# Optimization experiments

Measured on AMD Instinct MI355X. Metric: run time of the kernel, lower is better.

The kernel has to match this reference:

```python
import jax, jax.numpy as jnp
import numpy as np

KSIZE = 31
PAD = KSIZE // 2  # 15
SIGMA = 6.0
GAMMA_0 = 1.0
GAMMA_DELTA = 0.6
THRESH = 55.0


def _gabor_kernels(theta, freq):
    """Per-pixel spatially-varying Gabor kernels.
    theta, freq: [N] -> kernels [N, KSIZE, KSIZE].
    Frequency is chirped along the wave axis by freq_delta = freq/3 and the
    Gaussian aspect ratio varies from gamma_0 at the center by gamma_delta
    toward the kernel edge (matches generate_custom_gabor_torch semantics).
    """
    half = KSIZE // 2
    r = jnp.arange(-half, half + 1, dtype=jnp.float32)
    yy, xx = jnp.meshgrid(r, r, indexing='ij')  # [K,K]
    ct = jnp.cos(theta)[:, None, None]
    st = jnp.sin(theta)[:, None, None]
    x_t = xx * ct + yy * st       # along-wave coordinate
    y_t = -xx * st + yy * ct      # across-wave coordinate
    f0 = freq[:, None, None]
    f_local = f0 + (f0 / 3.0) * (y_t / half)          # freq_delta = freq/3
    gamma = GAMMA_0 + GAMMA_DELTA * jnp.abs(y_t) / half
    env = jnp.exp(-(x_t ** 2 + (gamma * y_t) ** 2) / (2.0 * SIGMA ** 2))
    return env * jnp.cos(2.0 * jnp.pi * f_local * x_t)


def _gabor_forward(fprint, freq_map, theta_map):
    H, W = fprint.shape
    i0, i1 = PAD, H - 16          # loop bounds: range(15, H-16)
    j0, j1 = PAD, W - 16
    Hout, Wout = i1 - i0, j1 - j0  # H-31, W-31 (patches always fully in-bounds)

    # [K*K, H-30, W-30] im2col patches; valid-output index 0 is center PAD.
    patches = jax.lax.conv_general_dilated_patches(
        fprint[None, None], (KSIZE, KSIZE), (1, 1), 'VALID')[0]
    patches = patches[:, :Hout, :Wout]  # centers i0..i1-1, j0..j1-1

    theta = theta_map[i0:i1, j0:j1].astype(jnp.float32) / 180.0 * jnp.pi
    freq = 0.025 + 0.0015 * freq_map[i0:i1, j0:j1].astype(jnp.float32)
    kernels = _gabor_kernels(theta.reshape(-1), freq.reshape(-1))
    kernels = kernels.reshape(Hout, Wout, KSIZE * KSIZE)

    vals = jnp.einsum('khw,hwk->hw', patches, kernels)
    out = fprint.at[i0:i1, j0:j1].set(vals)

    # normalize2Df_print_torch: shift min to 0, scale max to 100
    out = out - jnp.min(out)
    mx = jnp.max(out)
    out = jnp.where(mx != 0, out / mx * 100.0, out)
    # binarize2Df_print_torch
    return jnp.where(out > THRESH, 100.0, 0.0)


def setup_inputs() -> dict:
    key = jax.random.key(0)
    k1, k2, k3 = jax.random.split(key, 3)
    H = W = 320
    fprint = jax.random.uniform(k1, (H, W), dtype=jnp.float32) * 100.0
    freq_map = jax.random.randint(k2, (H, W), 0, 20, dtype=jnp.int32)
    theta_map = jax.random.randint(k3, (H, W), 0, 180, dtype=jnp.int32)
    return {"fprint": fprint, "freq_map": freq_map, "theta_map": theta_map}


def reference(fprint, freq_map, theta_map):
    return _gabor_forward(fprint, freq_map, theta_map)
```

## Files before the change

### kernel.cpp

```cpp
#include <hip/hip_runtime.h>
#include <math.h>

#define KS    31
#define KSP   32
#define PADV  15
#define IMG   320
#define NOUT  289
#define NTH   180
#define TABQ  (KSP * KSP)

#define PBX   4
#define PBY   2
#define TROWS (PBY + KSP - 1)
#define TSTR  37
#define NSTG  (TROWS * TSTR)
#define GX    73
#define GY    145
#define NPART (GX * GY)
#define NBORD 18879

typedef float f32x4 __attribute__((ext_vector_type(4)));

__global__ __launch_bounds__(256) void build_eftab(float2* __restrict__ tab) {
    const int t = blockIdx.x >> 2;
    const int e = (blockIdx.x & 3) * 256 + threadIdx.x;
    const float th = ((float)t / 180.0f) * 3.14159265358979323846f;
    float st, ct;
    sincosf(th, &st, &ct);
    int dy = e >> 5, dx = e & 31;
    float2 v = make_float2(0.0f, 0.0f);
    if (dy < KS && dx < KS) {
        float y = (float)(dy - PADV);
        float x = (float)(dx - PADV);
        float x_t = fmaf(x,  ct, y * st);
        float y_t = fmaf(-x, st, y * ct);
        float gamma = fmaf(0.04f, fabsf(y_t), 1.0f);
        float gyt = gamma * y_t;
        float env = expf(-fmaf(x_t, x_t, gyt * gyt) * (1.0f / 72.0f));
        float phi = fmaf(x_t * y_t, (1.0f / 45.0f), x_t);
        v = make_float2(env, phi);
    }
    tab[(size_t)t * TABQ + e] = v;
}

__global__ __launch_bounds__(256, 4) void gabor_conv(
    const float* __restrict__ fp, const int* __restrict__ fmap,
    const int* __restrict__ tmap, const float2* __restrict__ tab,
    float* __restrict__ out, float2* __restrict__ part)
{
    __shared__ float tile[NSTG];
    __shared__ float smin[8], smax[8];
    const int bh = blockIdx.y * PBY;
    const int bw = blockIdx.x * PBX;
    const int tid = threadIdx.x;

    const int wave = tid >> 6, lane = tid & 63;
    const int half = lane >> 5, l = lane & 31;
    const int lr = l & 15, lh = l >> 4;
    const int pb  = wave * 2 + half;
    const int pxl = pb & 3, pyl = pb >> 2;
    const int oy = bh + pyl, ox = bw + pxl;
    const bool valid = (oy < NOUT) && (ox < NOUT);

    f32x4 g0a, g0b, g0c, g0d, g1a, g1b, g1c, g1d;
    f32x4 g2a, g2b, g2c, g2d, g3a, g3b, g3c, g3d;
    float f0 = 0.0f;
    unsigned long long a = 0;

#define ISSUE(R0,R1,R2,R3,A,O0,O1,O2,O3) asm volatile(                        \
        "global_load_dwordx4 %0, %4, off offset:" #O0 "\n\t"                  \
        "global_load_dwordx4 %1, %4, off offset:" #O1 "\n\t"                  \
        "global_load_dwordx4 %2, %4, off offset:" #O2 "\n\t"                  \
        "global_load_dwordx4 %3, %4, off offset:" #O3                         \
        : "=&v"(R0), "=&v"(R1), "=&v"(R2), "=&v"(R3) : "v"(A) : "memory")
#define WAITTIE(N,R0,R1,R2,R3)                                                \
        asm volatile("s_waitcnt vmcnt(" #N ")"                                \
            : "+v"(R0), "+v"(R1), "+v"(R2), "+v"(R3) :: "memory");            \
        __builtin_amdgcn_sched_barrier(0)
#define WAITTIE8(R0,R1,R2,R3,R4,R5,R6,R7)                                     \
        asm volatile("s_waitcnt vmcnt(8)"                                     \
            : "+v"(R0), "+v"(R1), "+v"(R2), "+v"(R3),                         \
              "+v"(R4), "+v"(R5), "+v"(R6), "+v"(R7) :: "memory");            \
        __builtin_amdgcn_sched_barrier(0)
#define COMP(W, i) { const float* tr_ = tbase + 2 * (i) * TSTR;               \
        float w0_ = W.x * __builtin_amdgcn_cosf(f0 * W.y);                    \
        float w1_ = W.z * __builtin_amdgcn_cosf(f0 * W.w);                    \
        acc0 = fmaf(tr_[0], w0_, acc0); acc1 = fmaf(tr_[1], w1_, acc1); }

    if (valid) {
        const int iy = oy + PADV, ix = ox + PADV;
        const int theta = tmap[iy * IMG + ix];
        f0 = 0.025f + 0.0015f * (float)fmap[iy * IMG + ix];
        a = (unsigned long long)(tab + (size_t)theta * TABQ) + (size_t)l * 16;
        ISSUE(g0a,g0b,g0c,g0d, a, 0,    512,  1024, 1536);
        ISSUE(g1a,g1b,g1c,g1d, a, 2048, 2560, 3072, 3584);
    }

    for (int i = tid; i < NSTG; i += 256) {
        int r = i / TSTR, c = i - r * TSTR;
        int gr = bh + r, gc = bw + c;
        tile[i] = (gr < IMG && gc < IMG) ? fp[gr * IMG + gc] : 0.0f;
    }
    __syncthreads();

    float acc0 = 0.0f, acc1 = 0.0f;
    if (valid) {
        unsigned long long a2 = a + 4096;
        const float* tbase = &tile[(pyl + lh) * TSTR + pxl + 2 * lr];

        ISSUE(g2a,g2b,g2c,g2d, a2, 0,    512,  1024, 1536);
        ISSUE(g3a,g3b,g3c,g3d, a2, 2048, 2560, 3072, 3584);
        WAITTIE8(g0a,g0b,g0c,g0d,g1a,g1b,g1c,g1d);
        COMP(g0a, 0) COMP(g0b, 1) COMP(g0c, 2) COMP(g0d, 3)
        COMP(g1a, 4) COMP(g1b, 5) COMP(g1c, 6) COMP(g1d, 7)
        __builtin_amdgcn_sched_barrier(0);
        WAITTIE(4, g2a,g2b,g2c,g2d);
        COMP(g2a, 8) COMP(g2b, 9) COMP(g2c, 10) COMP(g2d, 11)
        __builtin_amdgcn_sched_barrier(0);
        WAITTIE(0, g3a,g3b,g3c,g3d);
        COMP(g3a, 12) COMP(g3b, 13) COMP(g3c, 14) COMP(g3d, 15)
    }
#undef COMP
#undef WAITTIE8
#undef WAITTIE
#undef ISSUE

    float v = acc0 + acc1;
    v += __shfl_xor(v, 1, 64);
    v += __shfl_xor(v, 2, 64);
    v += __shfl_xor(v, 4, 64);
    v += __shfl_xor(v, 8, 64);
    v += __shfl_xor(v, 16, 64);

    if (l == 0) {
        smin[pb] = valid ? v : INFINITY;
        smax[pb] = valid ? v : -INFINITY;
        if (valid) out[(oy + PADV) * IMG + (ox + PADV)] = v;
    }
    __syncthreads();
    if (tid == 0) {
        float mn = smin[0], mx = smax[0];
        #pragma unroll
        for (int k = 1; k < 8; ++k) {
            mn = fminf(mn, smin[k]);
            mx = fmaxf(mx, smax[k]);
        }
        part[blockIdx.y * GX + blockIdx.x] = make_float2(mn, mx);
    }
}

__global__ __launch_bounds__(1024) void reduce_final(
    const float2* __restrict__ part, const float* __restrict__ fp,
    float* __restrict__ mm)
{
    __shared__ float smin[16], smax[16];
    float vmin = INFINITY, vmax = -INFINITY;
    for (int i = threadIdx.x; i < NPART; i += 1024) {
        float2 p = part[i];
        vmin = fminf(vmin, p.x);
        vmax = fmaxf(vmax, p.y);
    }
    for (int t = threadIdx.x; t < NBORD; t += 1024) {
        int p;
        if (t < 4800) {
            p = t;
        } else if (t < 9920) {
            int s = t - 4800;
            p = (304 + s / 320) * 320 + (s % 320);
        } else {
            int s = t - 9920;
            int r = 15 + s / 31, c = s % 31;
            int col = (c < 15) ? c : 289 + c;
            p = r * 320 + col;
        }
        float v = fp[p];
        vmin = fminf(vmin, v);
        vmax = fmaxf(vmax, v);
    }
    for (int off = 32; off; off >>= 1) {
        vmin = fminf(vmin, __shfl_down(vmin, off, 64));
        vmax = fmaxf(vmax, __shfl_down(vmax, off, 64));
    }
    const int wave = threadIdx.x >> 6;
    if ((threadIdx.x & 63) == 0) { smin[wave] = vmin; smax[wave] = vmax; }
    __syncthreads();
    if (threadIdx.x == 0) {
        float mn = smin[0], mx = smax[0];
        #pragma unroll
        for (int k = 1; k < 16; ++k) {
            mn = fminf(mn, smin[k]);
            mx = fmaxf(mx, smax[k]);
        }
        mm[0] = mn;
        mm[1] = mx;
    }
}

__global__ __launch_bounds__(256) void finalize(
    const float* __restrict__ fp, float* __restrict__ out,
    const float* __restrict__ mm)
{
    int p = blockIdx.x * 256 + threadIdx.x;
    if (p >= IMG * IMG) return;
    int i = p / IMG, j = p - i * IMG;
    bool inner = (i >= PADV) && (i < PADV + NOUT) && (j >= PADV) && (j < PADV + NOUT);
    float raw = inner ? out[p] : fp[p];
    float mn = mm[0];
    float mx = mm[1] - mn;
    float v  = raw - mn;
    if (mx != 0.0f) v = v / mx * 100.0f;
    out[p] = (v > 55.0f) ? 100.0f : 0.0f;
}

extern "C" void kernel_launch(void* const* d_in, const int* in_sizes, int n_in,
                              void* d_out, int out_size, void* d_ws, size_t ws_size,
                              hipStream_t stream) {
    const float* fp   = (const float*)d_in[0];
    const int*   fmap = (const int*)d_in[1];
    const int*   tmap = (const int*)d_in[2];
    float* out = (float*)d_out;

    float*  mm   = (float*)d_ws;
    float2* part = (float2*)((char*)d_ws + 256);
    float2* tab  = (float2*)((char*)d_ws + 131072);

    hipLaunchKernelGGL(build_eftab, dim3(NTH * 4), dim3(256), 0, stream, tab);

    hipLaunchKernelGGL(gabor_conv, dim3(GX, GY), dim3(256), 0, stream,
                       fp, fmap, tmap, tab, out, part);

    hipLaunchKernelGGL(reduce_final, dim3(1), dim3(1024), 0, stream, part, fp, mm);

    int nblk = (IMG * IMG + 255) / 256;
    hipLaunchKernelGGL(finalize, dim3(nblk), dim3(256), 0, stream, fp, out, mm);
}
```

Measured before the change: 51.61 us.

## Vectorize tile staging and reorder table loads after barrier

Stages the image tile with 16-byte vector loads into a 33x40 padded layout, clamping edge reads instead of zero-filling them. All table loads for a thread are now issued after the tile barrier, each group waited on separately, rather than overlapping half of them with staging. Launch bounds drop from 4 to 2 blocks per CU, which allows more registers per thread but may lower occupancy. This gives up the earlier overlap of table-load latency with tile staging in exchange for fewer, wider staging loads.

```diff
diff --git a/kernel.cpp b/kernel.cpp
--- a/kernel.cpp
+++ b/kernel.cpp
@@ -11,9 +11,10 @@
 
 #define PBX   4
 #define PBY   2
-#define TROWS (PBY + KSP - 1)
-#define TSTR  37
+#define TROWS 33
+#define TSTR  40
 #define NSTG  (TROWS * TSTR)
+#define NQ    330
 #define GX    73
 #define GY    145
 #define NPART (GX * GY)
@@ -43,7 +44,7 @@
     tab[(size_t)t * TABQ + e] = v;
 }
 
-__global__ __launch_bounds__(256, 4) void gabor_conv(
+__global__ __launch_bounds__(256, 2) void gabor_conv(
     const float* __restrict__ fp, const int* __restrict__ fmap,
     const int* __restrict__ tmap, const float2* __restrict__ tab,
     float* __restrict__ out, float2* __restrict__ part)
@@ -54,6 +55,18 @@
     const int bw = blockIdx.x * PBX;
     const int tid = threadIdx.x;
 
+    #pragma unroll
+    for (int pass = 0; pass < 2; ++pass) {
+        int s = pass * 256 + tid;
+        if (pass == 0 || s < NQ) {
+            int r = s / 10, q = s - r * 10;
+            int gr = bh + r;      if (gr > IMG - 1) gr = IMG - 1;
+            int gc = bw + 4 * q;  if (gc > IMG - 4) gc = IMG - 4;
+            *(f32x4*)&tile[s * 4] = *(const f32x4*)(fp + gr * IMG + gc);
+        }
+    }
+    __syncthreads();
+
     const int wave = tid >> 6, lane = tid & 63;
     const int half = lane >> 5, l = lane & 31;
     const int lr = l & 15, lh = l >> 4;
@@ -62,10 +75,20 @@
     const int oy = bh + pyl, ox = bw + pxl;
     const bool valid = (oy < NOUT) && (ox < NOUT);
 
-    f32x4 g0a, g0b, g0c, g0d, g1a, g1b, g1c, g1d;
-    f32x4 g2a, g2b, g2c, g2d, g3a, g3b, g3c, g3d;
-    float f0 = 0.0f;
-    unsigned long long a = 0;
+    float acc0 = 0.0f, acc1 = 0.0f;
+    if (valid) {
+        const int iy = oy + PADV, ix = ox + PADV;
+        const int theta = tmap[iy * IMG + ix];
+        float f0 = 0.025f + 0.0015f * (float)fmap[iy * IMG + ix];
+        asm volatile("" : "+v"(f0));
+
+        unsigned long long a  =
+            (unsigned long long)(tab + (size_t)theta * TABQ) + (size_t)l * 16;
+        unsigned long long a2 = a + 4096;
+        const float* tbase = &tile[(pyl + lh) * TSTR + pxl + 2 * lr];
+
+        f32x4 g0a, g0b, g0c, g0d, g1a, g1b, g1c, g1d;
+        f32x4 g2a, g2b, g2c, g2d, g3a, g3b, g3c, g3d;
 
 #define ISSUE(R0,R1,R2,R3,A,O0,O1,O2,O3) asm volatile(                        \
         "global_load_dwordx4 %0, %4, off offset:" #O0 "\n\t"                  \
@@ -77,41 +100,19 @@
         asm volatile("s_waitcnt vmcnt(" #N ")"                                \
             : "+v"(R0), "+v"(R1), "+v"(R2), "+v"(R3) :: "memory");            \
         __builtin_amdgcn_sched_barrier(0)
-#define WAITTIE8(R0,R1,R2,R3,R4,R5,R6,R7)                                     \
-        asm volatile("s_waitcnt vmcnt(8)"                                     \
-            : "+v"(R0), "+v"(R1), "+v"(R2), "+v"(R3),                         \
-              "+v"(R4), "+v"(R5), "+v"(R6), "+v"(R7) :: "memory");            \
-        __builtin_amdgcn_sched_barrier(0)
 #define COMP(W, i) { const float* tr_ = tbase + 2 * (i) * TSTR;               \
         float w0_ = W.x * __builtin_amdgcn_cosf(f0 * W.y);                    \
         float w1_ = W.z * __builtin_amdgcn_cosf(f0 * W.w);                    \
         acc0 = fmaf(tr_[0], w0_, acc0); acc1 = fmaf(tr_[1], w1_, acc1); }
 
-    if (valid) {
-        const int iy = oy + PADV, ix = ox + PADV;
-        const int theta = tmap[iy * IMG + ix];
-        f0 = 0.025f + 0.0015f * (float)fmap[iy * IMG + ix];
-        a = (unsigned long long)(tab + (size_t)theta * TABQ) + (size_t)l * 16;
-        ISSUE(g0a,g0b,g0c,g0d, a, 0,    512,  1024, 1536);
-        ISSUE(g1a,g1b,g1c,g1d, a, 2048, 2560, 3072, 3584);
-    }
-
-    for (int i = tid; i < NSTG; i += 256) {
-        int r = i / TSTR, c = i - r * TSTR;
-        int gr = bh + r, gc = bw + c;
-        tile[i] = (gr < IMG && gc < IMG) ? fp[gr * IMG + gc] : 0.0f;
-    }
-    __syncthreads();
-
-    float acc0 = 0.0f, acc1 = 0.0f;
-    if (valid) {
-        unsigned long long a2 = a + 4096;
-        const float* tbase = &tile[(pyl + lh) * TSTR + pxl + 2 * lr];
-
+        ISSUE(g0a,g0b,g0c,g0d, a,  0,    512,  1024, 1536);
+        ISSUE(g1a,g1b,g1c,g1d, a,  2048, 2560, 3072, 3584);
         ISSUE(g2a,g2b,g2c,g2d, a2, 0,    512,  1024, 1536);
         ISSUE(g3a,g3b,g3c,g3d, a2, 2048, 2560, 3072, 3584);
-        WAITTIE8(g0a,g0b,g0c,g0d,g1a,g1b,g1c,g1d);
+        WAITTIE(12, g0a,g0b,g0c,g0d);
         COMP(g0a, 0) COMP(g0b, 1) COMP(g0c, 2) COMP(g0d, 3)
+        __builtin_amdgcn_sched_barrier(0);
+        WAITTIE(8, g1a,g1b,g1c,g1d);
         COMP(g1a, 4) COMP(g1b, 5) COMP(g1c, 6) COMP(g1d, 7)
         __builtin_amdgcn_sched_barrier(0);
         WAITTIE(4, g2a,g2b,g2c,g2d);
@@ -119,11 +120,10 @@
         __builtin_amdgcn_sched_barrier(0);
         WAITTIE(0, g3a,g3b,g3c,g3d);
         COMP(g3a, 12) COMP(g3b, 13) COMP(g3c, 14) COMP(g3d, 15)
-    }
 #undef COMP
-#undef WAITTIE8
 #undef WAITTIE
 #undef ISSUE
+    }
 
     float v = acc0 + acc1;
     v += __shfl_xor(v, 1, 64);
```

New measurement: 48.71 us. 5.6% less time.
